# Optimization experiments

Measured on AMD Instinct MI355X. Metric: run time of the kernel, lower is better.

Reference implementation:

```python
import jax, jax.numpy as jnp
import numpy as np

B, S, D, H = 4, 2048, 1024, 16
HD = D // H  # head_dim = 64


def setup_inputs() -> dict:
    key = jax.random.key(0)
    ks = jax.random.split(key, 11)
    scale = 1.0 / np.sqrt(D)
    q = jax.random.normal(ks[0], (B, S, D), jnp.float32)
    k = jax.random.normal(ks[1], (B, S, D), jnp.float32)
    v = jax.random.normal(ks[2], (B, S, D), jnp.float32)
    # causal mask, broadcastable over [B, H, Sq, Sk]
    mask = jnp.tril(jnp.ones((S, S), bool))[None, None, :, :]
    Wq = jax.random.normal(ks[3], (D, D), jnp.float32) * scale
    bq = jnp.zeros((D,), jnp.float32)
    Wk = jax.random.normal(ks[4], (D, D), jnp.float32) * scale
    bk = jnp.zeros((D,), jnp.float32)
    Wv = jax.random.normal(ks[5], (D, D), jnp.float32) * scale
    bv = jnp.zeros((D,), jnp.float32)
    Wo = jax.random.normal(ks[6], (D, D), jnp.float32) * scale
    bo = jnp.zeros((D,), jnp.float32)
    return {"q": q, "k": k, "v": v, "mask": mask,
            "Wq": Wq, "bq": bq, "Wk": Wk, "bk": bk,
            "Wv": Wv, "bv": bv, "Wo": Wo, "bo": bo}


def reference(q, k, v, mask, Wq, bq, Wk, bk, Wv, bv, Wo, bo):
    b, sq, _ = q.shape
    sk = k.shape[1]
    # projections (torch Linear: x @ W.T + b)
    qh = (q @ Wq.T + bq).reshape(b, sq, H, HD)
    kh = (k @ Wk.T + bk).reshape(b, sk, H, HD)
    vh = (v @ Wv.T + bv).reshape(b, sk, H, HD)
    # scaled dot-product attention: [b, h, sq, sk]
    scores = jnp.einsum('bqhd,bkhd->bhqk', qh, kh) / jnp.sqrt(jnp.float32(HD))
    scores = jnp.where(mask, scores, jnp.float32(-jnp.inf))
    attn = jax.nn.softmax(scores, axis=-1)
    out = jnp.einsum('bhqk,bkhd->bqhd', attn, vh).reshape(b, sq, D)
    return out @ Wo.T + bo
```

## Files before the change

kernel.cpp:

```cpp
#include <hip/hip_runtime.h>
#include <hip/hip_bf16.h>
#include <cstdint>
#include <cstddef>

typedef __attribute__((ext_vector_type(4))) float f32x4;
typedef __attribute__((ext_vector_type(16))) float f32x16;
typedef __attribute__((ext_vector_type(8))) __bf16 bf16x8;

constexpr int Bc = 4, Sc = 2048, Dc = 1024, Hc = 16, HDc = 64;
constexpr int Mrows = Bc * Sc;
constexpr int Kdim = Dc;

__device__ __forceinline__ void gload_lds16(const void* g, void* lds) {
  __builtin_amdgcn_global_load_lds(
      (const __attribute__((address_space(1))) void*)g,
      (__attribute__((address_space(3))) void*)lds, 16, 0, 0);
}

__global__ void cvt4_f32_to_bf16(const float* __restrict__ s0, const float* __restrict__ s1,
                                 const float* __restrict__ s2, const float* __restrict__ s3,
                                 __bf16* __restrict__ d0, __bf16* __restrict__ d1,
                                 __bf16* __restrict__ d2, __bf16* __restrict__ d3, int n4each) {
  int i = blockIdx.x * blockDim.x + threadIdx.x;
  int which = i / n4each, j = i - which * n4each;
  const float* s = which == 0 ? s0 : which == 1 ? s1 : which == 2 ? s2 : s3;
  __bf16* d = which == 0 ? d0 : which == 1 ? d1 : which == 2 ? d2 : d3;
  float4 f = ((const float4*)s)[j];
  union { __bf16 h[4]; uint2 u; } p;
  p.h[0] = (__bf16)f.x; p.h[1] = (__bf16)f.y;
  p.h[2] = (__bf16)f.z; p.h[3] = (__bf16)f.w;
  ((uint2*)d)[j] = p.u;
}

__global__ __launch_bounds__(256, 2)
void gemm_qkv(const float* __restrict__ qin, const float* __restrict__ kin,
              const float* __restrict__ vin, const __bf16* __restrict__ Wcat,
              const float* __restrict__ bq, const float* __restrict__ bk,
              const float* __restrict__ bv,
              __bf16* __restrict__ Qh, __bf16* __restrict__ Kh,
              __bf16* __restrict__ Vt, float qscale)
{
  __shared__ __align__(16) __bf16 As[128 * 32];
  __shared__ __align__(16) __bf16 Bs[128 * 32];
  const int tid = threadIdx.x;
  const int wave = tid >> 6, lane = tid & 63;
  const int wr = wave >> 1, wc = wave & 1;
  const int r = lane & 15, hi = lane >> 4;
  const int lin = (int)blockIdx.y * 24 + (int)blockIdx.x;
  const int xcd = lin & 7, s8 = lin >> 3;
  const int my = (xcd << 3) | (s8 / 24);
  const int mx = s8 % 24;
  const int m0 = my * 128, n0 = mx * 128;
  const int proj = n0 >> 10;
  const float* Xa = proj == 0 ? qin : proj == 1 ? kin : vin;

  f32x4 acc[4][4] = {};

  for (int k0 = 0; k0 < Kdim; k0 += 32) {
    #pragma unroll
    for (int c = 0; c < 2; ++c) {
      int chunk = c * 256 + tid;
      int row = chunk >> 2;
      int cw = chunk & 3;
      int hc = cw ^ (row & 3);
      const float* src = Xa + (size_t)(m0 + row) * Kdim + k0 + hc * 8;
      float4 f0 = *(const float4*)src;
      float4 f1 = *(const float4*)(src + 4);
      union { __bf16 h[8]; uint4 u; } pk;
      pk.h[0] = (__bf16)f0.x; pk.h[1] = (__bf16)f0.y;
      pk.h[2] = (__bf16)f0.z; pk.h[3] = (__bf16)f0.w;
      pk.h[4] = (__bf16)f1.x; pk.h[5] = (__bf16)f1.y;
      pk.h[6] = (__bf16)f1.z; pk.h[7] = (__bf16)f1.w;
      *(uint4*)&As[(size_t)chunk * 8] = pk.u;
    }
    #pragma unroll
    for (int c = 0; c < 2; ++c) {
      int chunk = c * 256 + wave * 64 + lane;
      int row = chunk >> 2;
      int hc = (chunk & 3) ^ (row & 3);
      gload_lds16(Wcat + (size_t)(n0 + row) * Kdim + k0 + hc * 8,
                  &Bs[(size_t)(c * 256 + wave * 64) * 8]);
    }
    __syncthreads();
    bf16x8 af[4], bfr[4];
    #pragma unroll
    for (int m = 0; m < 4; ++m) {
      int rowl = wr * 64 + m * 16 + r;
      af[m] = *(const bf16x8*)&As[rowl * 32 + ((hi ^ (rowl & 3)) * 8)];
    }
    #pragma unroll
    for (int n = 0; n < 4; ++n) {
      int rowl = wc * 64 + n * 16 + r;
      bfr[n] = *(const bf16x8*)&Bs[rowl * 32 + ((hi ^ (rowl & 3)) * 8)];
    }
    #pragma unroll
    for (int m = 0; m < 4; ++m)
      #pragma unroll
      for (int n = 0; n < 4; ++n)
        acc[m][n] = __builtin_amdgcn_mfma_f32_16x16x32_bf16(af[m], bfr[n], acc[m][n], 0, 0, 0);
    __syncthreads();
  }

  const float* bias = proj == 0 ? bq : proj == 1 ? bk : bv;
  if (proj < 2) {
    __bf16* out = proj == 0 ? Qh : Kh;
    const float sc = proj == 0 ? qscale : 1.0f;
    #pragma unroll
    for (int m = 0; m < 4; ++m)
      #pragma unroll
      for (int n = 0; n < 4; ++n)
        #pragma unroll
        for (int rg = 0; rg < 4; ++rg) {
          int row_g = m0 + wr * 64 + m * 16 + hi * 4 + rg;
          int col_g = n0 + wc * 64 + n * 16 + r;
          int c = col_g & 1023, h = c >> 6, d = c & 63;
          int b = row_g >> 11, s = row_g & (Sc - 1);
          float v = (acc[m][n][rg] + bias[c]) * sc;
          out[((((size_t)b * Hc + h) * Sc + s) << 6) + d] = (__bf16)v;
        }
  } else {
    #pragma unroll
    for (int m = 0; m < 4; ++m)
      #pragma unroll
      for (int n = 0; n < 4; ++n) {
        int row0 = m0 + wr * 64 + m * 16 + hi * 4;
        int col_g = n0 + wc * 64 + n * 16 + r;
        int c = col_g & 1023, h = c >> 6, d = c & 63;
        int b = row0 >> 11, s = row0 & (Sc - 1);
        union { __bf16 hh[4]; uint2 u; } w;
        #pragma unroll
        for (int rg = 0; rg < 4; ++rg)
          w.hh[rg] = (__bf16)(acc[m][n][rg] + bias[c]);
        *(uint2*)&Vt[((((size_t)b * Hc + h) * HDc + d) << 11) + s] = w.u;
      }
  }
}

__global__ __launch_bounds__(256, 2)
void gemm_out(const __bf16* __restrict__ A, const __bf16* __restrict__ Bw,
              const float* __restrict__ bias, float* __restrict__ outp)
{
  __shared__ __align__(16) __bf16 As[128 * 32];
  __shared__ __align__(16) __bf16 Bs[128 * 32];
  const int tid = threadIdx.x;
  const int wave = tid >> 6, lane = tid & 63;
  const int wr = wave >> 1, wc = wave & 1;
  const int r = lane & 15, hi = lane >> 4;
  const int lin = (int)blockIdx.y * 8 + (int)blockIdx.x;
  const int xcd = lin & 7, s8 = lin >> 3;
  const int m0 = (((xcd << 3) | (s8 >> 3)) ) * 128;
  const int n0 = (s8 & 7) * 128;

  f32x4 acc[4][4] = {};

  for (int k0 = 0; k0 < Kdim; k0 += 32) {
    #pragma unroll
    for (int c = 0; c < 2; ++c) {
      int chunk = c * 256 + wave * 64 + lane;
      int row = chunk >> 2;
      int hc = (chunk & 3) ^ (row & 3);
      gload_lds16(A  + (size_t)(m0 + row) * Kdim + k0 + hc * 8,
                  &As[(size_t)(c * 256 + wave * 64) * 8]);
      gload_lds16(Bw + (size_t)(n0 + row) * Kdim + k0 + hc * 8,
                  &Bs[(size_t)(c * 256 + wave * 64) * 8]);
    }
    __syncthreads();
    bf16x8 af[4], bfr[4];
    #pragma unroll
    for (int m = 0; m < 4; ++m) {
      int rowl = wr * 64 + m * 16 + r;
      af[m] = *(const bf16x8*)&As[rowl * 32 + ((hi ^ (rowl & 3)) * 8)];
    }
    #pragma unroll
    for (int n = 0; n < 4; ++n) {
      int rowl = wc * 64 + n * 16 + r;
      bfr[n] = *(const bf16x8*)&Bs[rowl * 32 + ((hi ^ (rowl & 3)) * 8)];
    }
    #pragma unroll
    for (int m = 0; m < 4; ++m)
      #pragma unroll
      for (int n = 0; n < 4; ++n)
        acc[m][n] = __builtin_amdgcn_mfma_f32_16x16x32_bf16(af[m], bfr[n], acc[m][n], 0, 0, 0);
    __syncthreads();
  }

  #pragma unroll
  for (int m = 0; m < 4; ++m)
    #pragma unroll
    for (int n = 0; n < 4; ++n)
      #pragma unroll
      for (int rg = 0; rg < 4; ++rg) {
        int row_g = m0 + wr * 64 + m * 16 + hi * 4 + rg;
        int col_g = n0 + wc * 64 + n * 16 + r;
        outp[(size_t)row_g * Dc + col_g] = acc[m][n][rg] + bias[col_g];
      }
}

__global__ __launch_bounds__(128, 2)
void attn_causal(const __bf16* __restrict__ Qh, const __bf16* __restrict__ Kh,
                 const __bf16* __restrict__ Vt, __bf16* __restrict__ outp)
{
  const int tid = threadIdx.x;
  const int wave = tid >> 6, lane = tid & 63;
  const int c32 = lane & 31;
  const int h5 = lane >> 5;
  const int lin = (int)blockIdx.y * 32 + (int)blockIdx.x;
  const int xcd = lin & 7, s8 = lin >> 3;
  const int bh = (xcd << 3) | (s8 >> 5);
  const int px = s8 & 31;
  const int qh = wave ? (63 - px) : px;
  const int q0 = qh * 32;
  const __bf16* Q = Qh + (size_t)bh * (Sc * HDc);
  const __bf16* K = Kh + (size_t)bh * (Sc * HDc);
  const __bf16* V = Vt + (size_t)bh * (HDc * Sc);

  bf16x8 qf[4];
  #pragma unroll
  for (int dc = 0; dc < 4; ++dc)
    qf[dc] = *(const bf16x8*)&Q[(size_t)(q0 + c32) * 64 + dc * 16 + h5 * 8];

  f32x16 o0 = {}, o1 = {};
  float mrow = -1e30f, lrow = 0.f;

  const int T = qh + 1;
  bf16x8 kf[4], vf0[2], vf1[2];

  #pragma unroll
  for (int dc = 0; dc < 4; ++dc)
    kf[dc] = *(const bf16x8*)&K[(size_t)c32 * 64 + dc * 16 + h5 * 8];
  #pragma unroll
  for (int kc = 0; kc < 2; ++kc) {
    vf0[kc] = *(const bf16x8*)&V[(size_t)c32 * Sc + kc * 16 + h5 * 8];
    vf1[kc] = *(const bf16x8*)&V[(size_t)(32 + c32) * Sc + kc * 16 + h5 * 8];
  }

  for (int t = 0; t < T; ++t) {
    const bool diag = (t == T - 1);
    const int kvn = (t + 1) * 32;

    f32x16 sn = {};
    __builtin_amdgcn_s_setprio(1);
    sn = __builtin_amdgcn_mfma_f32_32x32x16_bf16(kf[0], qf[0], sn, 0, 0, 0);
    sn = __builtin_amdgcn_mfma_f32_32x32x16_bf16(kf[1], qf[1], sn, 0, 0, 0);
    sn = __builtin_amdgcn_mfma_f32_32x32x16_bf16(kf[2], qf[2], sn, 0, 0, 0);
    sn = __builtin_amdgcn_mfma_f32_32x32x16_bf16(kf[3], qf[3], sn, 0, 0, 0);
    __builtin_amdgcn_s_setprio(0);

    if (diag) {
      #pragma unroll
      for (int reg = 0; reg < 16; ++reg)
        if ((reg & 3) + 8 * (reg >> 2) + 4 * h5 > c32) sn[reg] = -1e30f;
    }

    float mx = fmaxf(fmaxf(fmaxf(sn[0], sn[1]), fmaxf(sn[2], sn[3])),
                     fmaxf(fmaxf(sn[4], sn[5]), fmaxf(sn[6], sn[7])));
    mx = fmaxf(mx, fmaxf(fmaxf(fmaxf(sn[8], sn[9]), fmaxf(sn[10], sn[11])),
                         fmaxf(fmaxf(sn[12], sn[13]), fmaxf(sn[14], sn[15]))));
    mx = fmaxf(mx, __shfl_xor(mx, 32));
    if (__any(mx > mrow + 8.f)) {
      float mnew = fmaxf(mrow, mx);
      float sc = __builtin_exp2f(mrow - mnew);
      lrow *= sc;
      o0 *= sc;
      o1 *= sc;
      mrow = mnew;
    }
    float rs = 0.f;
    #pragma unroll
    for (int reg = 0; reg < 16; ++reg) {
      float p = __builtin_exp2f(sn[reg] - mrow);
      sn[reg] = p;
      rs += p;
    }
    rs += __shfl_xor(rs, 32);
    lrow += rs;

    uint32_t u0, u1, u2, u3, u4, u5, u6, u7;
    asm("v_cvt_pk_bf16_f32 %0, %1, %2" : "=v"(u0) : "v"(sn[0]),  "v"(sn[1]));
    asm("v_cvt_pk_bf16_f32 %0, %1, %2" : "=v"(u1) : "v"(sn[2]),  "v"(sn[3]));
    asm("v_cvt_pk_bf16_f32 %0, %1, %2" : "=v"(u2) : "v"(sn[4]),  "v"(sn[5]));
    asm("v_cvt_pk_bf16_f32 %0, %1, %2" : "=v"(u3) : "v"(sn[6]),  "v"(sn[7]));
    asm("v_cvt_pk_bf16_f32 %0, %1, %2" : "=v"(u4) : "v"(sn[8]),  "v"(sn[9]));
    asm("v_cvt_pk_bf16_f32 %0, %1, %2" : "=v"(u5) : "v"(sn[10]), "v"(sn[11]));
    asm("v_cvt_pk_bf16_f32 %0, %1, %2" : "=v"(u6) : "v"(sn[12]), "v"(sn[13]));
    asm("v_cvt_pk_bf16_f32 %0, %1, %2" : "=v"(u7) : "v"(sn[14]), "v"(sn[15]));
    asm("v_permlane32_swap_b32 %0, %1" : "+v"(u0), "+v"(u2));
    asm("v_permlane32_swap_b32 %0, %1" : "+v"(u1), "+v"(u3));
    asm("v_permlane32_swap_b32 %0, %1" : "+v"(u4), "+v"(u6));
    asm("v_permlane32_swap_b32 %0, %1" : "+v"(u5), "+v"(u7));
    union { uint32_t w[4]; bf16x8 v; } pb0, pb1;
    pb0.w[0] = u0; pb0.w[1] = u1; pb0.w[2] = u2; pb0.w[3] = u3;
    pb1.w[0] = u4; pb1.w[1] = u5; pb1.w[2] = u6; pb1.w[3] = u7;

    if (t + 1 < T) {
      #pragma unroll
      for (int dc = 0; dc < 4; ++dc)
        kf[dc] = *(const bf16x8*)&K[(size_t)(kvn + c32) * 64 + dc * 16 + h5 * 8];
    }

    __builtin_amdgcn_s_setprio(1);
    o0 = __builtin_amdgcn_mfma_f32_32x32x16_bf16(vf0[0], pb0.v, o0, 0, 0, 0);
    o0 = __builtin_amdgcn_mfma_f32_32x32x16_bf16(vf0[1], pb1.v, o0, 0, 0, 0);
    o1 = __builtin_amdgcn_mfma_f32_32x32x16_bf16(vf1[0], pb0.v, o1, 0, 0, 0);
    o1 = __builtin_amdgcn_mfma_f32_32x32x16_bf16(vf1[1], pb1.v, o1, 0, 0, 0);
    __builtin_amdgcn_s_setprio(0);

    if (t + 1 < T) {
      #pragma unroll
      for (int kc = 0; kc < 2; ++kc) {
        vf0[kc] = *(const bf16x8*)&V[(size_t)c32 * Sc + kvn + kc * 16 + h5 * 8];
        vf1[kc] = *(const bf16x8*)&V[(size_t)(32 + c32) * Sc + kvn + kc * 16 + h5 * 8];
      }
    }
  }

  const int b = bh >> 4, h = bh & 15;
  const float inv = 1.f / lrow;
  __bf16* obase = outp + ((size_t)b * Sc + q0 + c32) * Dc + h * 64;
  #pragma unroll
  for (int rq = 0; rq < 4; ++rq) {
    union { __bf16 hh[4]; uint2 u; } w;
    #pragma unroll
    for (int rr = 0; rr < 4; ++rr) w.hh[rr] = (__bf16)(o0[rq * 4 + rr] * inv);
    *(uint2*)&obase[rq * 8 + h5 * 4] = w.u;
  }
  #pragma unroll
  for (int rq = 0; rq < 4; ++rq) {
    union { __bf16 hh[4]; uint2 u; } w;
    #pragma unroll
    for (int rr = 0; rr < 4; ++rr) w.hh[rr] = (__bf16)(o1[rq * 4 + rr] * inv);
    *(uint2*)&obase[32 + rq * 8 + h5 * 4] = w.u;
  }
}

extern "C" void kernel_launch(void* const* d_in, const int* in_sizes, int n_in,
                              void* d_out, int out_size, void* d_ws, size_t ws_size,
                              hipStream_t stream) {
  const float* q  = (const float*)d_in[0];
  const float* k  = (const float*)d_in[1];
  const float* v  = (const float*)d_in[2];
  const float* Wq = (const float*)d_in[4];
  const float* bq = (const float*)d_in[5];
  const float* Wk = (const float*)d_in[6];
  const float* bk = (const float*)d_in[7];
  const float* Wv = (const float*)d_in[8];
  const float* bv = (const float*)d_in[9];
  const float* Wo = (const float*)d_in[10];
  const float* bo = (const float*)d_in[11];

  char* ws = (char*)d_ws;
  constexpr size_t MB = 1u << 20;
  __bf16* Wcat = (__bf16*)(ws + 0 * MB);
  __bf16* Wkb  = (__bf16*)(ws + 2 * MB);
  __bf16* Wvb  = (__bf16*)(ws + 4 * MB);
  __bf16* Wob  = (__bf16*)(ws + 6 * MB);
  __bf16* Xbf  = (__bf16*)(ws + 8 * MB);
  __bf16* QhB  = (__bf16*)(ws + 24 * MB);
  __bf16* KhB  = (__bf16*)(ws + 40 * MB);
  __bf16* VtB  = (__bf16*)(ws + 56 * MB);

  const int nW4 = (Dc * Dc) / 4;
  cvt4_f32_to_bf16<<<(4 * nW4) / 256, 256, 0, stream>>>(Wq, Wk, Wv, Wo, Wcat, Wkb, Wvb, Wob, nW4);

  const float qscale = 0.125f * 1.44269504f;
  gemm_qkv<<<dim3(24, Mrows / 128), 256, 0, stream>>>(q, k, v, Wcat, bq, bk, bv,
                                                      QhB, KhB, VtB, qscale);

  attn_causal<<<dim3(32, Bc * Hc), 128, 0, stream>>>(QhB, KhB, VtB, Xbf);

  gemm_out<<<dim3(8, Mrows / 128), 256, 0, stream>>>(Xbf, Wob, bo, (float*)d_out);
}
```

Measured before the change: 238.4 us.

## Split causal attention KV range across two waves and merge partial softmax

Each block now handles one 32-row query tile, with its two waves splitting the KV tiles in half and merging partial softmax state (max, sum, output) through shared memory. This replaces pairing a short and a long query tile per block. The grid doubles and blocks are ordered longest tile first. It also swaps exp2f for raw v_exp_f32 and issues the next K load earlier, which adds LDS traffic, a barrier and a merge step per block.

```diff
diff --git a/kernel.cpp b/kernel.cpp
--- a/kernel.cpp
+++ b/kernel.cpp
@@ -15,6 +15,12 @@
   __builtin_amdgcn_global_load_lds(
       (const __attribute__((address_space(1))) void*)g,
       (__attribute__((address_space(3))) void*)lds, 16, 0, 0);
+}
+
+__device__ __forceinline__ float exp2_fast(float x) {
+  float r;
+  asm("v_exp_f32 %0, %1" : "=v"(r) : "v"(x));
+  return r;
 }
 
 __global__ void cvt4_f32_to_bf16(const float* __restrict__ s0, const float* __restrict__ s1,
@@ -200,15 +206,18 @@
 void attn_causal(const __bf16* __restrict__ Qh, const __bf16* __restrict__ Kh,
                  const __bf16* __restrict__ Vt, __bf16* __restrict__ outp)
 {
+  __shared__ float OaS[32][64];
+  __shared__ float MS[64];
+  __shared__ float LS[64];
+
   const int tid = threadIdx.x;
   const int wave = tid >> 6, lane = tid & 63;
   const int c32 = lane & 31;
   const int h5 = lane >> 5;
-  const int lin = (int)blockIdx.y * 32 + (int)blockIdx.x;
+  const int lin = (int)blockIdx.y * 64 + (int)blockIdx.x;
   const int xcd = lin & 7, s8 = lin >> 3;
-  const int bh = (xcd << 3) | (s8 >> 5);
-  const int px = s8 & 31;
-  const int qh = wave ? (63 - px) : px;
+  const int bh = (xcd << 3) | (s8 >> 6);
+  const int qh = 63 - (s8 & 63);
   const int q0 = qh * 32;
   const __bf16* Q = Qh + (size_t)bh * (Sc * HDc);
   const __bf16* K = Kh + (size_t)bh * (Sc * HDc);
@@ -223,18 +232,22 @@
   float mrow = -1e30f, lrow = 0.f;
 
   const int T = qh + 1;
+  const int half = (T + 1) >> 1;
+  const int t0 = wave ? half : 0;
+  const int t1 = wave ? T : half;
+
   bf16x8 kf[4], vf0[2], vf1[2];
 
   #pragma unroll
   for (int dc = 0; dc < 4; ++dc)
-    kf[dc] = *(const bf16x8*)&K[(size_t)c32 * 64 + dc * 16 + h5 * 8];
+    kf[dc] = *(const bf16x8*)&K[(size_t)(t0 * 32 + c32) * 64 + dc * 16 + h5 * 8];
   #pragma unroll
   for (int kc = 0; kc < 2; ++kc) {
-    vf0[kc] = *(const bf16x8*)&V[(size_t)c32 * Sc + kc * 16 + h5 * 8];
-    vf1[kc] = *(const bf16x8*)&V[(size_t)(32 + c32) * Sc + kc * 16 + h5 * 8];
-  }
-
-  for (int t = 0; t < T; ++t) {
+    vf0[kc] = *(const bf16x8*)&V[(size_t)c32 * Sc + t0 * 32 + kc * 16 + h5 * 8];
+    vf1[kc] = *(const bf16x8*)&V[(size_t)(32 + c32) * Sc + t0 * 32 + kc * 16 + h5 * 8];
+  }
+
+  for (int t = t0; t < t1; ++t) {
     const bool diag = (t == T - 1);
     const int kvn = (t + 1) * 32;
 
@@ -246,6 +259,12 @@
     sn = __builtin_amdgcn_mfma_f32_32x32x16_bf16(kf[3], qf[3], sn, 0, 0, 0);
     __builtin_amdgcn_s_setprio(0);
 
+    if (t + 1 < t1) {
+      #pragma unroll
+      for (int dc = 0; dc < 4; ++dc)
+        kf[dc] = *(const bf16x8*)&K[(size_t)(kvn + c32) * 64 + dc * 16 + h5 * 8];
+    }
+
     if (diag) {
       #pragma unroll
       for (int reg = 0; reg < 16; ++reg)
@@ -259,7 +278,7 @@
     mx = fmaxf(mx, __shfl_xor(mx, 32));
     if (__any(mx > mrow + 8.f)) {
       float mnew = fmaxf(mrow, mx);
-      float sc = __builtin_exp2f(mrow - mnew);
+      float sc = exp2_fast(mrow - mnew);
       lrow *= sc;
       o0 *= sc;
       o1 *= sc;
@@ -268,7 +287,7 @@
     float rs = 0.f;
     #pragma unroll
     for (int reg = 0; reg < 16; ++reg) {
-      float p = __builtin_exp2f(sn[reg] - mrow);
+      float p = exp2_fast(sn[reg] - mrow);
       sn[reg] = p;
       rs += p;
     }
@@ -292,12 +311,6 @@
     pb0.w[0] = u0; pb0.w[1] = u1; pb0.w[2] = u2; pb0.w[3] = u3;
     pb1.w[0] = u4; pb1.w[1] = u5; pb1.w[2] = u6; pb1.w[3] = u7;
 
-    if (t + 1 < T) {
-      #pragma unroll
-      for (int dc = 0; dc < 4; ++dc)
-        kf[dc] = *(const bf16x8*)&K[(size_t)(kvn + c32) * 64 + dc * 16 + h5 * 8];
-    }
-
     __builtin_amdgcn_s_setprio(1);
     o0 = __builtin_amdgcn_mfma_f32_32x32x16_bf16(vf0[0], pb0.v, o0, 0, 0, 0);
     o0 = __builtin_amdgcn_mfma_f32_32x32x16_bf16(vf0[1], pb1.v, o0, 0, 0, 0);
@@ -305,7 +318,7 @@
     o1 = __builtin_amdgcn_mfma_f32_32x32x16_bf16(vf1[1], pb1.v, o1, 0, 0, 0);
     __builtin_amdgcn_s_setprio(0);
 
-    if (t + 1 < T) {
+    if (t + 1 < t1) {
       #pragma unroll
       for (int kc = 0; kc < 2; ++kc) {
         vf0[kc] = *(const bf16x8*)&V[(size_t)c32 * Sc + kvn + kc * 16 + h5 * 8];
@@ -314,22 +327,41 @@
     }
   }
 
-  const int b = bh >> 4, h = bh & 15;
-  const float inv = 1.f / lrow;
-  __bf16* obase = outp + ((size_t)b * Sc + q0 + c32) * Dc + h * 64;
-  #pragma unroll
-  for (int rq = 0; rq < 4; ++rq) {
-    union { __bf16 hh[4]; uint2 u; } w;
-    #pragma unroll
-    for (int rr = 0; rr < 4; ++rr) w.hh[rr] = (__bf16)(o0[rq * 4 + rr] * inv);
-    *(uint2*)&obase[rq * 8 + h5 * 4] = w.u;
-  }
-  #pragma unroll
-  for (int rq = 0; rq < 4; ++rq) {
-    union { __bf16 hh[4]; uint2 u; } w;
-    #pragma unroll
-    for (int rr = 0; rr < 4; ++rr) w.hh[rr] = (__bf16)(o1[rq * 4 + rr] * inv);
-    *(uint2*)&obase[32 + rq * 8 + h5 * 4] = w.u;
+  if (wave == 1) {
+    MS[lane] = mrow;
+    LS[lane] = lrow;
+    #pragma unroll
+    for (int reg = 0; reg < 16; ++reg) {
+      OaS[reg][lane] = o0[reg];
+      OaS[16 + reg][lane] = o1[reg];
+    }
+  }
+  __syncthreads();
+  if (wave == 0) {
+    float mB = MS[lane], lB = LS[lane];
+    float mF = fmaxf(mrow, mB);
+    float aA = __builtin_exp2f(mrow - mF);
+    float aB = __builtin_exp2f(mB - mF);
+    float inv = 1.f / (lrow * aA + lB * aB);
+
+    const int b = bh >> 4, h = bh & 15;
+    __bf16* obase = outp + ((size_t)b * Sc + q0 + c32) * Dc + h * 64;
+    #pragma unroll
+    for (int rq = 0; rq < 4; ++rq) {
+      union { __bf16 hh[4]; uint2 u; } w;
+      #pragma unroll
+      for (int rr = 0; rr < 4; ++rr)
+        w.hh[rr] = (__bf16)((o0[rq * 4 + rr] * aA + OaS[rq * 4 + rr][lane] * aB) * inv);
+      *(uint2*)&obase[rq * 8 + h5 * 4] = w.u;
+    }
+    #pragma unroll
+    for (int rq = 0; rq < 4; ++rq) {
+      union { __bf16 hh[4]; uint2 u; } w;
+      #pragma unroll
+      for (int rr = 0; rr < 4; ++rr)
+        w.hh[rr] = (__bf16)((o1[rq * 4 + rr] * aA + OaS[16 + rq * 4 + rr][lane] * aB) * inv);
+      *(uint2*)&obase[32 + rq * 8 + h5 * 4] = w.u;
+    }
   }
 }
 
@@ -366,7 +398,7 @@
   gemm_qkv<<<dim3(24, Mrows / 128), 256, 0, stream>>>(q, k, v, Wcat, bq, bk, bv,
                                                       QhB, KhB, VtB, qscale);
 
-  attn_causal<<<dim3(32, Bc * Hc), 128, 0, stream>>>(QhB, KhB, VtB, Xbf);
+  attn_causal<<<dim3(64, Bc * Hc), 128, 0, stream>>>(QhB, KhB, VtB, Xbf);
 
   gemm_out<<<dim3(8, Mrows / 128), 256, 0, stream>>>(Xbf, Wob, bo, (float*)d_out);
 }
```

After: 257.2 us. 7.9% more time.

## Process two KV tiles per iteration in attention loop and use raw v_exp

Applied to the files above, without the earlier changes.

The attention inner loop now handles two 32-key tiles per iteration, interleaving their QK MFMAs and sharing one max/rescale step, with double-sized register prefetch of K and V. When the tile count is odd, a phantom tile is loaded from a clamped index and masked to -inf. exp2 calls are replaced with an inline v_exp_f32 to avoid the libm wrapper. This gives more independent MFMA work to hide latency and halves the softmax bookkeeping, at the cost of more registers and possibly lower occupancy.

```diff
diff --git a/kernel.cpp b/kernel.cpp
--- a/kernel.cpp
+++ b/kernel.cpp
@@ -15,6 +15,12 @@
   __builtin_amdgcn_global_load_lds(
       (const __attribute__((address_space(1))) void*)g,
       (__attribute__((address_space(3))) void*)lds, 16, 0, 0);
+}
+
+__device__ __forceinline__ float exp2_fast(float x) {
+  float r;
+  asm("v_exp_f32 %0, %1" : "=v"(r) : "v"(x));
+  return r;
 }
 
 __global__ void cvt4_f32_to_bf16(const float* __restrict__ s0, const float* __restrict__ s1,
@@ -223,93 +229,140 @@
   float mrow = -1e30f, lrow = 0.f;
 
   const int T = qh + 1;
-  bf16x8 kf[4], vf0[2], vf1[2];
-
-  #pragma unroll
-  for (int dc = 0; dc < 4; ++dc)
-    kf[dc] = *(const bf16x8*)&K[(size_t)c32 * 64 + dc * 16 + h5 * 8];
-  #pragma unroll
-  for (int kc = 0; kc < 2; ++kc) {
-    vf0[kc] = *(const bf16x8*)&V[(size_t)c32 * Sc + kc * 16 + h5 * 8];
-    vf1[kc] = *(const bf16x8*)&V[(size_t)(32 + c32) * Sc + kc * 16 + h5 * 8];
-  }
-
-  for (int t = 0; t < T; ++t) {
-    const bool diag = (t == T - 1);
-    const int kvn = (t + 1) * 32;
-
-    f32x16 sn = {};
+  bf16x8 kfA[4], kfB[4], vA0[2], vA1[2], vB0[2], vB1[2];
+
+  {
+    const int tb = (T > 1) ? 1 : 0;
+    #pragma unroll
+    for (int dc = 0; dc < 4; ++dc) {
+      kfA[dc] = *(const bf16x8*)&K[(size_t)c32 * 64 + dc * 16 + h5 * 8];
+      kfB[dc] = *(const bf16x8*)&K[(size_t)(tb * 32 + c32) * 64 + dc * 16 + h5 * 8];
+    }
+    #pragma unroll
+    for (int kc = 0; kc < 2; ++kc) {
+      vA0[kc] = *(const bf16x8*)&V[(size_t)c32 * Sc + kc * 16 + h5 * 8];
+      vA1[kc] = *(const bf16x8*)&V[(size_t)(32 + c32) * Sc + kc * 16 + h5 * 8];
+      vB0[kc] = *(const bf16x8*)&V[(size_t)c32 * Sc + tb * 32 + kc * 16 + h5 * 8];
+      vB1[kc] = *(const bf16x8*)&V[(size_t)(32 + c32) * Sc + tb * 32 + kc * 16 + h5 * 8];
+    }
+  }
+
+  for (int t = 0; t < T; t += 2) {
+    const bool diagA = (t == T - 1);
+    const bool diagB = (t + 1 == T - 1);
+    const bool phantomB = (t + 1 >= T);
+
+    f32x16 snA = {}, snB = {};
     __builtin_amdgcn_s_setprio(1);
-    sn = __builtin_amdgcn_mfma_f32_32x32x16_bf16(kf[0], qf[0], sn, 0, 0, 0);
-    sn = __builtin_amdgcn_mfma_f32_32x32x16_bf16(kf[1], qf[1], sn, 0, 0, 0);
-    sn = __builtin_amdgcn_mfma_f32_32x32x16_bf16(kf[2], qf[2], sn, 0, 0, 0);
-    sn = __builtin_amdgcn_mfma_f32_32x32x16_bf16(kf[3], qf[3], sn, 0, 0, 0);
+    snA = __builtin_amdgcn_mfma_f32_32x32x16_bf16(kfA[0], qf[0], snA, 0, 0, 0);
+    snB = __builtin_amdgcn_mfma_f32_32x32x16_bf16(kfB[0], qf[0], snB, 0, 0, 0);
+    snA = __builtin_amdgcn_mfma_f32_32x32x16_bf16(kfA[1], qf[1], snA, 0, 0, 0);
+    snB = __builtin_amdgcn_mfma_f32_32x32x16_bf16(kfB[1], qf[1], snB, 0, 0, 0);
+    snA = __builtin_amdgcn_mfma_f32_32x32x16_bf16(kfA[2], qf[2], snA, 0, 0, 0);
+    snB = __builtin_amdgcn_mfma_f32_32x32x16_bf16(kfB[2], qf[2], snB, 0, 0, 0);
+    snA = __builtin_amdgcn_mfma_f32_32x32x16_bf16(kfA[3], qf[3], snA, 0, 0, 0);
+    snB = __builtin_amdgcn_mfma_f32_32x32x16_bf16(kfB[3], qf[3], snB, 0, 0, 0);
     __builtin_amdgcn_s_setprio(0);
 
-    if (diag) {
+    if (t + 2 < T) {
+      const int tbn = (t + 3 < T) ? (t + 3) : (T - 1);
+      #pragma unroll
+      for (int dc = 0; dc < 4; ++dc) {
+        kfA[dc] = *(const bf16x8*)&K[(size_t)((t + 2) * 32 + c32) * 64 + dc * 16 + h5 * 8];
+        kfB[dc] = *(const bf16x8*)&K[(size_t)(tbn * 32 + c32) * 64 + dc * 16 + h5 * 8];
+      }
+    }
+
+    if (diagA) {
       #pragma unroll
       for (int reg = 0; reg < 16; ++reg)
-        if ((reg & 3) + 8 * (reg >> 2) + 4 * h5 > c32) sn[reg] = -1e30f;
-    }
-
-    float mx = fmaxf(fmaxf(fmaxf(sn[0], sn[1]), fmaxf(sn[2], sn[3])),
-                     fmaxf(fmaxf(sn[4], sn[5]), fmaxf(sn[6], sn[7])));
-    mx = fmaxf(mx, fmaxf(fmaxf(fmaxf(sn[8], sn[9]), fmaxf(sn[10], sn[11])),
-                         fmaxf(fmaxf(sn[12], sn[13]), fmaxf(sn[14], sn[15]))));
+        if ((reg & 3) + 8 * (reg >> 2) + 4 * h5 > c32) snA[reg] = -1e30f;
+    }
+    if (diagB) {
+      #pragma unroll
+      for (int reg = 0; reg < 16; ++reg)
+        if ((reg & 3) + 8 * (reg >> 2) + 4 * h5 > c32) snB[reg] = -1e30f;
+    } else if (phantomB) {
+      #pragma unroll
+      for (int reg = 0; reg < 16; ++reg) snB[reg] = -1e30f;
+    }
+
+    float mx = fmaxf(fmaxf(fmaxf(snA[0], snA[1]), fmaxf(snA[2], snA[3])),
+                     fmaxf(fmaxf(snA[4], snA[5]), fmaxf(snA[6], snA[7])));
+    mx = fmaxf(mx, fmaxf(fmaxf(fmaxf(snA[8], snA[9]), fmaxf(snA[10], snA[11])),
+                         fmaxf(fmaxf(snA[12], snA[13]), fmaxf(snA[14], snA[15]))));
+    mx = fmaxf(mx, fmaxf(fmaxf(fmaxf(snB[0], snB[1]), fmaxf(snB[2], snB[3])),
+                         fmaxf(fmaxf(snB[4], snB[5]), fmaxf(snB[6], snB[7]))));
+    mx = fmaxf(mx, fmaxf(fmaxf(fmaxf(snB[8], snB[9]), fmaxf(snB[10], snB[11])),
+                         fmaxf(fmaxf(snB[12], snB[13]), fmaxf(snB[14], snB[15]))));
     mx = fmaxf(mx, __shfl_xor(mx, 32));
     if (__any(mx > mrow + 8.f)) {
       float mnew = fmaxf(mrow, mx);
-      float sc = __builtin_exp2f(mrow - mnew);
-      lrow *= sc;
-      o0 *= sc;
-      o1 *= sc;
-      mrow = mnew;
+      float sc = exp2_fast(mrow - mnew);
+      lrow *= sc; o0 *= sc; o1 *= sc; mrow = mnew;
     }
     float rs = 0.f;
     #pragma unroll
     for (int reg = 0; reg < 16; ++reg) {
-      float p = __builtin_exp2f(sn[reg] - mrow);
-      sn[reg] = p;
-      rs += p;
+      float pa = exp2_fast(snA[reg] - mrow);
+      float pb = exp2_fast(snB[reg] - mrow);
+      snA[reg] = pa; snB[reg] = pb;
+      rs += pa + pb;
     }
     rs += __shfl_xor(rs, 32);
     lrow += rs;
 
-    uint32_t u0, u1, u2, u3, u4, u5, u6, u7;
-    asm("v_cvt_pk_bf16_f32 %0, %1, %2" : "=v"(u0) : "v"(sn[0]),  "v"(sn[1]));
-    asm("v_cvt_pk_bf16_f32 %0, %1, %2" : "=v"(u1) : "v"(sn[2]),  "v"(sn[3]));
-    asm("v_cvt_pk_bf16_f32 %0, %1, %2" : "=v"(u2) : "v"(sn[4]),  "v"(sn[5]));
-    asm("v_cvt_pk_bf16_f32 %0, %1, %2" : "=v"(u3) : "v"(sn[6]),  "v"(sn[7]));
-    asm("v_cvt_pk_bf16_f32 %0, %1, %2" : "=v"(u4) : "v"(sn[8]),  "v"(sn[9]));
-    asm("v_cvt_pk_bf16_f32 %0, %1, %2" : "=v"(u5) : "v"(sn[10]), "v"(sn[11]));
-    asm("v_cvt_pk_bf16_f32 %0, %1, %2" : "=v"(u6) : "v"(sn[12]), "v"(sn[13]));
-    asm("v_cvt_pk_bf16_f32 %0, %1, %2" : "=v"(u7) : "v"(sn[14]), "v"(sn[15]));
-    asm("v_permlane32_swap_b32 %0, %1" : "+v"(u0), "+v"(u2));
-    asm("v_permlane32_swap_b32 %0, %1" : "+v"(u1), "+v"(u3));
-    asm("v_permlane32_swap_b32 %0, %1" : "+v"(u4), "+v"(u6));
-    asm("v_permlane32_swap_b32 %0, %1" : "+v"(u5), "+v"(u7));
-    union { uint32_t w[4]; bf16x8 v; } pb0, pb1;
-    pb0.w[0] = u0; pb0.w[1] = u1; pb0.w[2] = u2; pb0.w[3] = u3;
-    pb1.w[0] = u4; pb1.w[1] = u5; pb1.w[2] = u6; pb1.w[3] = u7;
-
-    if (t + 1 < T) {
-      #pragma unroll
-      for (int dc = 0; dc < 4; ++dc)
-        kf[dc] = *(const bf16x8*)&K[(size_t)(kvn + c32) * 64 + dc * 16 + h5 * 8];
-    }
+    uint32_t a0, a1, a2, a3, a4, a5, a6, a7;
+    uint32_t b0, b1, b2, b3, b4, b5, b6, b7;
+    asm("v_cvt_pk_bf16_f32 %0, %1, %2" : "=v"(a0) : "v"(snA[0]),  "v"(snA[1]));
+    asm("v_cvt_pk_bf16_f32 %0, %1, %2" : "=v"(a1) : "v"(snA[2]),  "v"(snA[3]));
+    asm("v_cvt_pk_bf16_f32 %0, %1, %2" : "=v"(a2) : "v"(snA[4]),  "v"(snA[5]));
+    asm("v_cvt_pk_bf16_f32 %0, %1, %2" : "=v"(a3) : "v"(snA[6]),  "v"(snA[7]));
+    asm("v_cvt_pk_bf16_f32 %0, %1, %2" : "=v"(a4) : "v"(snA[8]),  "v"(snA[9]));
+    asm("v_cvt_pk_bf16_f32 %0, %1, %2" : "=v"(a5) : "v"(snA[10]), "v"(snA[11]));
+    asm("v_cvt_pk_bf16_f32 %0, %1, %2" : "=v"(a6) : "v"(snA[12]), "v"(snA[13]));
+    asm("v_cvt_pk_bf16_f32 %0, %1, %2" : "=v"(a7) : "v"(snA[14]), "v"(snA[15]));
+    asm("v_cvt_pk_bf16_f32 %0, %1, %2" : "=v"(b0) : "v"(snB[0]),  "v"(snB[1]));
+    asm("v_cvt_pk_bf16_f32 %0, %1, %2" : "=v"(b1) : "v"(snB[2]),  "v"(snB[3]));
+    asm("v_cvt_pk_bf16_f32 %0, %1, %2" : "=v"(b2) : "v"(snB[4]),  "v"(snB[5]));
+    asm("v_cvt_pk_bf16_f32 %0, %1, %2" : "=v"(b3) : "v"(snB[6]),  "v"(snB[7]));
+    asm("v_cvt_pk_bf16_f32 %0, %1, %2" : "=v"(b4) : "v"(snB[8]),  "v"(snB[9]));
+    asm("v_cvt_pk_bf16_f32 %0, %1, %2" : "=v"(b5) : "v"(snB[10]), "v"(snB[11]));
+    asm("v_cvt_pk_bf16_f32 %0, %1, %2" : "=v"(b6) : "v"(snB[12]), "v"(snB[13]));
+    asm("v_cvt_pk_bf16_f32 %0, %1, %2" : "=v"(b7) : "v"(snB[14]), "v"(snB[15]));
+    asm("v_permlane32_swap_b32 %0, %1" : "+v"(a0), "+v"(a2));
+    asm("v_permlane32_swap_b32 %0, %1" : "+v"(a1), "+v"(a3));
+    asm("v_permlane32_swap_b32 %0, %1" : "+v"(a4), "+v"(a6));
+    asm("v_permlane32_swap_b32 %0, %1" : "+v"(a5), "+v"(a7));
+    asm("v_permlane32_swap_b32 %0, %1" : "+v"(b0), "+v"(b2));
+    asm("v_permlane32_swap_b32 %0, %1" : "+v"(b1), "+v"(b3));
+    asm("v_permlane32_swap_b32 %0, %1" : "+v"(b4), "+v"(b6));
+    asm("v_permlane32_swap_b32 %0, %1" : "+v"(b5), "+v"(b7));
+    union { uint32_t w[4]; bf16x8 v; } pA0, pA1, pB0, pB1;
+    pA0.w[0] = a0; pA0.w[1] = a1; pA0.w[2] = a2; pA0.w[3] = a3;
+    pA1.w[0] = a4; pA1.w[1] = a5; pA1.w[2] = a6; pA1.w[3] = a7;
+    pB0.w[0] = b0; pB0.w[1] = b1; pB0.w[2] = b2; pB0.w[3] = b3;
+    pB1.w[0] = b4; pB1.w[1] = b5; pB1.w[2] = b6; pB1.w[3] = b7;
 
     __builtin_amdgcn_s_setprio(1);
-    o0 = __builtin_amdgcn_mfma_f32_32x32x16_bf16(vf0[0], pb0.v, o0, 0, 0, 0);
-    o0 = __builtin_amdgcn_mfma_f32_32x32x16_bf16(vf0[1], pb1.v, o0, 0, 0, 0);
-    o1 = __builtin_amdgcn_mfma_f32_32x32x16_bf16(vf1[0], pb0.v, o1, 0, 0, 0);
-    o1 = __builtin_amdgcn_mfma_f32_32x32x16_bf16(vf1[1], pb1.v, o1, 0, 0, 0);
+    o0 = __builtin_amdgcn_mfma_f32_32x32x16_bf16(vA0[0], pA0.v, o0, 0, 0, 0);
+    o1 = __builtin_amdgcn_mfma_f32_32x32x16_bf16(vA1[0], pA0.v, o1, 0, 0, 0);
+    o0 = __builtin_amdgcn_mfma_f32_32x32x16_bf16(vA0[1], pA1.v, o0, 0, 0, 0);
+    o1 = __builtin_amdgcn_mfma_f32_32x32x16_bf16(vA1[1], pA1.v, o1, 0, 0, 0);
+    o0 = __builtin_amdgcn_mfma_f32_32x32x16_bf16(vB0[0], pB0.v, o0, 0, 0, 0);
+    o1 = __builtin_amdgcn_mfma_f32_32x32x16_bf16(vB1[0], pB0.v, o1, 0, 0, 0);
+    o0 = __builtin_amdgcn_mfma_f32_32x32x16_bf16(vB0[1], pB1.v, o0, 0, 0, 0);
+    o1 = __builtin_amdgcn_mfma_f32_32x32x16_bf16(vB1[1], pB1.v, o1, 0, 0, 0);
     __builtin_amdgcn_s_setprio(0);
 
-    if (t + 1 < T) {
+    if (t + 2 < T) {
+      const int tbn = (t + 3 < T) ? (t + 3) : (T - 1);
       #pragma unroll
       for (int kc = 0; kc < 2; ++kc) {
-        vf0[kc] = *(const bf16x8*)&V[(size_t)c32 * Sc + kvn + kc * 16 + h5 * 8];
-        vf1[kc] = *(const bf16x8*)&V[(size_t)(32 + c32) * Sc + kvn + kc * 16 + h5 * 8];
+        vA0[kc] = *(const bf16x8*)&V[(size_t)c32 * Sc + (t + 2) * 32 + kc * 16 + h5 * 8];
+        vA1[kc] = *(const bf16x8*)&V[(size_t)(32 + c32) * Sc + (t + 2) * 32 + kc * 16 + h5 * 8];
+        vB0[kc] = *(const bf16x8*)&V[(size_t)c32 * Sc + tbn * 32 + kc * 16 + h5 * 8];
+        vB1[kc] = *(const bf16x8*)&V[(size_t)(32 + c32) * Sc + tbn * 32 + kc * 16 + h5 * 8];
       }
     }
   }
```

After: 253.0 us. +6.1%, slower.
